# Performance work log

Hardware: AMD Instinct MI355X
Metric: run time of the kernel (lower is better)

Reference implementation:

```python
import jax, jax.numpy as jnp
import numpy as np

EMBED_DIM = 1024
NUM_HEADS = 16
HEAD_DIM = EMBED_DIM // NUM_HEADS


def setup_inputs() -> dict:
    key = jax.random.key(0)
    ks = jax.random.split(key, 5)
    B, S, D = 2, 2048, EMBED_DIM
    scale = 1.0 / np.sqrt(D)
    x = jax.random.normal(ks[0], (B, S, D), dtype=jnp.float32)
    qkv_w = jax.random.uniform(ks[1], (3 * D, D), dtype=jnp.float32, minval=-scale, maxval=scale)
    qkv_b = jax.random.uniform(ks[2], (3 * D,), dtype=jnp.float32, minval=-scale, maxval=scale)
    out_w = jax.random.uniform(ks[3], (D, D), dtype=jnp.float32, minval=-scale, maxval=scale)
    out_b = jax.random.uniform(ks[4], (D,), dtype=jnp.float32, minval=-scale, maxval=scale)
    return {"x": x, "qkv_w": qkv_w, "qkv_b": qkv_b, "out_w": out_w, "out_b": out_b}


def reference(x, qkv_w, qkv_b, out_w, out_b):
    B, S, D = x.shape
    H, hd = NUM_HEADS, HEAD_DIM
    # QKV projection (torch Linear: y = x @ W^T + b)
    qkv = jnp.einsum('bsd,ed->bse', x, qkv_w) + qkv_b          # [B,S,3D]
    qkv = qkv.reshape(B, S, 3, H, hd)
    q, k, v = (jnp.moveaxis(qkv[:, :, i], 2, 1) for i in range(3))  # each [B,H,S,hd]
    scores = jnp.einsum('bhqd,bhkd->bhqk', q, k) / np.sqrt(hd)  # [B,H,S,S]
    probs = jax.nn.softmax(scores, axis=-1)
    attn = jnp.einsum('bhqk,bhkd->bhqd', probs, v)              # [B,H,S,hd]
    attn = jnp.moveaxis(attn, 1, 2).reshape(B, S, D)
    return jnp.einsum('bsd,ed->bse', attn, out_w) + out_b
```

## Files before the change

kernel.cpp:

```cpp
#include <hip/hip_runtime.h>
#include <stdint.h>

typedef __bf16 bf16;
typedef __attribute__((ext_vector_type(2))) __bf16 bf16x2;
typedef __attribute__((ext_vector_type(4))) __bf16 bf16x4;
typedef __attribute__((ext_vector_type(8))) __bf16 bf16x8;
typedef __attribute__((ext_vector_type(4))) float f32x4;
typedef __attribute__((ext_vector_type(16))) float f32x16;

#define LOG2E_OVER_8 0.18033688011112042f

#if __has_builtin(__builtin_amdgcn_exp2f)
#define EXP2(x) __builtin_amdgcn_exp2f(x)
#else
#define EXP2(x) exp2f(x)
#endif

__device__ __forceinline__ void gl_lds16(const bf16* g, bf16* l) {
  __builtin_amdgcn_global_load_lds(
      (const __attribute__((address_space(1))) void*)g,
      (__attribute__((address_space(3))) void*)l, 16, 0, 0);
}
#define WAIT_VM0_BARRIER() asm volatile("s_waitcnt vmcnt(0)\n\ts_barrier" ::: "memory")

__device__ __forceinline__ uint32_t pack2(float a, float b) {
  union { bf16x2 v; uint32_t u; } z;
  z.v[0] = (bf16)a; z.v[1] = (bf16)b;
  return z.u;
}

__device__ __forceinline__ void pl32swap(uint32_t& a, uint32_t& b) {
  asm("v_permlane32_swap_b32 %0, %1" : "+v"(a), "+v"(b));
}

#define N_X  (4096 * 1024)
#define N_WQ (3072 * 1024)
#define N_WO (1024 * 1024)
__global__ __launch_bounds__(256) void cvt3_kernel(const float* __restrict__ x,
                                                   const float* __restrict__ wq,
                                                   const float* __restrict__ wo,
                                                   bf16* __restrict__ d) {
  int i = (blockIdx.x * 256 + threadIdx.x) * 8;
  const float* s;
  if (i < N_X) s = x + i;
  else if (i < N_X + N_WQ) s = wq + (i - N_X);
  else s = wo + (i - N_X - N_WQ);
  float4 a = *(const float4*)s;
  float4 b = *(const float4*)(s + 4);
  bf16x8 o;
  o[0] = (bf16)a.x; o[1] = (bf16)a.y; o[2] = (bf16)a.z; o[3] = (bf16)a.w;
  o[4] = (bf16)b.x; o[5] = (bf16)b.y; o[6] = (bf16)b.z; o[7] = (bf16)b.w;
  *(bf16x8*)(d + i) = o;
}

template <int EPI>
__global__ __launch_bounds__(256, 3) void gemm_bt(
    const bf16* __restrict__ A, const bf16* __restrict__ Bw,
    const float* __restrict__ bias,
    bf16* __restrict__ qo, bf16* __restrict__ ko, bf16* __restrict__ vTo,
    float* __restrict__ outF) {
  constexpr int MT = EPI ? 64 : 128;
  constexpr int MI = MT / 32;
  constexpr int BK = EPI ? 64 : 32;
  constexpr int NC = BK / 32;
  constexpr int NIT = 1024 / BK;
  constexpr int ASZ = MT * BK;
  constexpr int BSZ = 128 * BK;
  constexpr int RS = 136;
  constexpr int SME0 = 2 * ASZ + 2 * BSZ;
  constexpr int SME = EPI ? SME0 : (SME0 > 128 * RS ? SME0 : 128 * RS);
  __shared__ __attribute__((aligned(16))) bf16 smem[SME];

  int bx, by;
  {
    const int f = blockIdx.x;
    const int xcd = f & 7, idx = f >> 3;
    if constexpr (EPI == 0) { by = xcd * 4 + (idx & 3); bx = idx >> 2; }
    else                    { by = xcd * 8 + (idx & 7); bx = idx >> 3; }
  }

  const int t = threadIdx.x;
  const int L = t & 63;
  const int li = L & 15;
  const int qd = L >> 4;
  const int w = t >> 6;
  const int wm = (w >> 1) * (MT / 2);
  const int wn = (w & 1) * 64;
  const int bm0 = by * MT;
  const int bn0 = bx * 128;
  const int r_st = t >> 2;
  const int c_st = (t & 3) * 8;

  const bf16* Ab = A + (size_t)bm0 * 1024;
  const bf16* Bb = Bw + (size_t)bn0 * 1024;

  auto issue = [&](int k0, int bi) {
    bf16* As_ = smem + bi * ASZ;
    bf16* Bs_ = smem + 2 * ASZ + bi * BSZ;
#pragma unroll
    for (int kc = 0; kc < NC; ++kc) {
      const int kk = k0 + kc * 32;
      gl_lds16(Ab + (size_t)r_st * 1024 + kk + c_st, As_ + kc * MT * 32 + t * 8);
      if constexpr (MT == 128)
        gl_lds16(Ab + (size_t)(r_st + 64) * 1024 + kk + c_st,
                 As_ + kc * MT * 32 + (t + 256) * 8);
      gl_lds16(Bb + (size_t)r_st * 1024 + kk + c_st, Bs_ + kc * 4096 + t * 8);
      gl_lds16(Bb + (size_t)(r_st + 64) * 1024 + kk + c_st,
               Bs_ + kc * 4096 + (t + 256) * 8);
    }
  };

  f32x4 acc[MI][4] = {};
  issue(0, 0);
  for (int it = 0; it < NIT; ++it) {
    WAIT_VM0_BARRIER();
    if (it < NIT - 1) issue((it + 1) * BK, (it + 1) & 1);
    const bf16* Ac = smem + (it & 1) * ASZ;
    const bf16* Bc = smem + 2 * ASZ + (it & 1) * BSZ;
#pragma unroll
    for (int kc = 0; kc < NC; ++kc) {
      const bf16* Ak = Ac + kc * MT * 32;
      const bf16* Bk = Bc + kc * 4096;
      bf16x8 af[MI], bfr[4];
#pragma unroll
      for (int mi = 0; mi < MI; ++mi)
        af[mi] = *(const bf16x8*)(Ak + (wm + mi * 16 + li) * 32 + qd * 8);
#pragma unroll
      for (int ni = 0; ni < 4; ++ni)
        bfr[ni] = *(const bf16x8*)(Bk + (wn + ni * 16 + li) * 32 + qd * 8);
#pragma unroll
      for (int mi = 0; mi < MI; ++mi)
#pragma unroll
        for (int ni = 0; ni < 4; ++ni)
          acc[mi][ni] = __builtin_amdgcn_mfma_f32_16x16x32_bf16(
              af[mi], bfr[ni], acc[mi][ni], 0, 0, 0);
    }
  }

  if constexpr (EPI == 0) {
    const int which = bn0 >> 10;
    __syncthreads();
    bf16* Ct = smem;
    if (which == 2) {
#pragma unroll
      for (int mi = 0; mi < MI; ++mi) {
        const int m_l = wm + mi * 16 + qd * 4;
#pragma unroll
        for (int ni = 0; ni < 4; ++ni) {
          const int n_l = wn + ni * 16 + li;
          const float bi = bias[bn0 + n_l];
          bf16x4 pk;
#pragma unroll
          for (int r = 0; r < 4; ++r) pk[r] = (bf16)(acc[mi][ni][r] + bi);
          *(bf16x4*)(Ct + n_l * RS + m_l) = pk;
        }
      }
    } else {
      const float sc = (which == 0) ? LOG2E_OVER_8 : 1.0f;
#pragma unroll
      for (int mi = 0; mi < MI; ++mi) {
        const int m_l = wm + mi * 16 + qd * 4;
#pragma unroll
        for (int ni = 0; ni < 4; ++ni) {
          const int n_l = wn + ni * 16 + li;
          const float bi = bias[bn0 + n_l];
#pragma unroll
          for (int r = 0; r < 4; ++r)
            Ct[(m_l + r) * RS + n_l] = (bf16)((acc[mi][ni][r] + bi) * sc);
        }
      }
    }
    __syncthreads();
    const int jr = t >> 4;
    const int jc = t & 15;
#pragma unroll
    for (int pass = 0; pass < 8; ++pass) {
      const int row = pass * 16 + jr;
      bf16x8 vv = *(const bf16x8*)(Ct + row * RS + jc * 8);
      if (which == 2) {
        const int n_g = bn0 + row;
        const int hh = (n_g >> 6) & 15, dd = n_g & 63;
        const int bb = bm0 >> 11;
        const int s_b = (bm0 & 2047) + jc * 8;
        *(bf16x8*)(vTo + ((size_t)(bb * 16 + hh) * 64 + dd) * 2048 + s_b) = vv;
      } else {
        const int m_g = bm0 + row;
        const int bb = m_g >> 11, ss = m_g & 2047;
        const int n_g = bn0 + jc * 8;
        const int hh = (n_g >> 6) & 15, dd = n_g & 63;
        bf16* dst = (which == 0 ? qo : ko);
        *(bf16x8*)(dst + ((size_t)(bb * 16 + hh) * 2048 + ss) * 64 + dd) = vv;
      }
    }
  } else {
#pragma unroll
    for (int mi = 0; mi < MI; ++mi) {
      const int m_g = bm0 + wm + mi * 16 + qd * 4;
#pragma unroll
      for (int ni = 0; ni < 4; ++ni) {
        const int n_g = bn0 + wn + ni * 16 + li;
        const float bi = bias[n_g];
#pragma unroll
        for (int r = 0; r < 4; ++r)
          outF[(size_t)(m_g + r) * 1024 + n_g] = acc[mi][ni][r] + bi;
      }
    }
  }
}

__global__ __launch_bounds__(512, 2) void attn_fwd(
    const bf16* __restrict__ Q, const bf16* __restrict__ K,
    const bf16* __restrict__ VT, bf16* __restrict__ AO) {
  __shared__ __attribute__((aligned(16))) bf16 smem[65536];
  const int t = threadIdx.x;
  const int half = t >> 8;
  const int tt = t & 255;
  const int L = t & 63;
  const int m31 = L & 31;
  const int hi = (L >> 5) & 1;
  const int w = (t >> 6) & 3;

  const int lid = blockIdx.x;
  const int bh_ = ((lid & 7) << 2) + (lid >> 6);
  const int qb = (lid >> 3) & 7;
  const int b = bh_ >> 4, h = bh_ & 15;
  const size_t bh = (size_t)(b * 16 + h);

  const bf16* Qp = Q + bh * 2048 * 64;
  const bf16* Kp = K + bh * 2048 * 64 + (size_t)half * 1024 * 64;
  const bf16* Vp = VT + bh * 64 * 2048 + half * 1024;
  const int q0 = qb * 256 + w * 64;

  bf16x8 qf[2][4];
#pragma unroll
  for (int qs = 0; qs < 2; ++qs)
#pragma unroll
    for (int s = 0; s < 4; ++s)
      qf[qs][s] = *(const bf16x8*)(
          Qp + (size_t)(q0 + qs * 32 + m31) * 64 + s * 16 + hi * 8);

  f32x16 acc[2][2] = {};
  f32x16 accS[2] = {};

  union FU { uint32_t u[4]; bf16x8 v; };
  FU onesf;
  onesf.u[0] = 0x3F803F80u; onesf.u[1] = 0x3F803F80u;
  onesf.u[2] = 0x3F803F80u; onesf.u[3] = 0x3F803F80u;

  bf16* Kbase = smem + half * 32768;
  bf16* Vbase = Kbase + 16384;

  const int srow = tt >> 3;
  const int scc = (tt & 7) ^ (srow & 7);
  auto issue = [&](int it2, int bi) {
#pragma unroll
    for (int tile = 0; tile < 2; ++tile) {
      const int kt = it2 * 2 + tile;
      const bf16* Kt = Kp + (size_t)kt * 4096;
      const bf16* Vt = Vp + kt * 64;
      bf16* Kd = Kbase + bi * 8192 + tile * 4096;
      bf16* Vd = Vbase + bi * 8192 + tile * 4096;
#pragma unroll
      for (int r = 0; r < 2; ++r) {
        gl_lds16(Kt + (srow + 32 * r) * 64 + scc * 8, Kd + (tt + 256 * r) * 8);
        gl_lds16(Vt + (size_t)(srow + 32 * r) * 2048 + scc * 8, Vd + (tt + 256 * r) * 8);
      }
    }
  };

  const int rlow = m31 & 7;

  auto SM = [&](const f32x16& st, FU* afp) {
    uint32_t pk[8];
#pragma unroll
    for (int j = 0; j < 8; ++j) {
      float a = EXP2(st[2 * j]);
      float c = EXP2(st[2 * j + 1]);
      pk[j] = pack2(a, c);
    }
    pl32swap(pk[0], pk[2]);
    pl32swap(pk[1], pk[3]);
    pl32swap(pk[4], pk[6]);
    pl32swap(pk[5], pk[7]);
    afp[0].u[0] = pk[0]; afp[0].u[1] = pk[1];
    afp[0].u[2] = pk[2]; afp[0].u[3] = pk[3];
    afp[1].u[0] = pk[4]; afp[1].u[1] = pk[5];
    afp[1].u[2] = pk[6]; afp[1].u[3] = pk[7];
  };

  issue(0, 0);
  for (int it2 = 0; it2 < 8; ++it2) {
    WAIT_VM0_BARRIER();
    if (it2 < 7) issue(it2 + 1, (it2 + 1) & 1);
    const bf16* Kc0 = Kbase + (it2 & 1) * 8192;
    const bf16* Vc0 = Vbase + (it2 & 1) * 8192;

    bf16x8 kfa[4][4];
#pragma unroll
    for (int kt = 0; kt < 4; ++kt)
#pragma unroll
      for (int s = 0; s < 4; ++s)
        kfa[kt][s] = *(const bf16x8*)(
            Kc0 + (kt >> 1) * 4096 +
            (((kt & 1) * 32 + m31) * 8 + ((2 * s + hi) ^ rlow)) * 8);
    __builtin_amdgcn_sched_barrier(0);

#pragma unroll
    for (int kt = 0; kt < 4; ++kt) {
      f32x16 st2[2];
      __builtin_amdgcn_s_setprio(1);
#pragma unroll
      for (int qs = 0; qs < 2; ++qs) {
        f32x16 z = {};
#pragma unroll
        for (int s = 0; s < 4; ++s)
          z = __builtin_amdgcn_mfma_f32_32x32x16_bf16(kfa[kt][s], qf[qs][s], z,
                                                      0, 0, 0);
        st2[qs] = z;
      }
      __builtin_amdgcn_s_setprio(0);

      bf16x8 vfa[2][2];
#pragma unroll
      for (int dt = 0; dt < 2; ++dt)
#pragma unroll
        for (int u = 0; u < 2; ++u)
          vfa[dt][u] = *(const bf16x8*)(
              Vc0 + (kt >> 1) * 4096 +
              ((dt * 32 + m31) * 8 + (((kt & 1) * 4 + u * 2 + hi) ^ rlow)) * 8);
      __builtin_amdgcn_sched_barrier(0);

      FU A[2][2];
      SM(st2[0], A[0]);
      SM(st2[1], A[1]);

      __builtin_amdgcn_s_setprio(1);
#pragma unroll
      for (int qs = 0; qs < 2; ++qs)
#pragma unroll
        for (int u = 0; u < 2; ++u)
          accS[qs] = __builtin_amdgcn_mfma_f32_32x32x16_bf16(
              A[qs][u].v, onesf.v, accS[qs], 0, 0, 0);
#pragma unroll
      for (int dt = 0; dt < 2; ++dt)
#pragma unroll
        for (int u = 0; u < 2; ++u)
#pragma unroll
          for (int qs = 0; qs < 2; ++qs)
            acc[dt][qs] = __builtin_amdgcn_mfma_f32_32x32x16_bf16(
                A[qs][u].v, vfa[dt][u], acc[dt][qs], 0, 0, 0);
      __builtin_amdgcn_s_setprio(0);
    }
  }

  __syncthreads();
  float* xch = (float*)smem;
  const int slot = w * 64 + L;
  float* rec = xch + (size_t)slot * 97;
  if (half == 1) {
#pragma unroll
    for (int dt = 0; dt < 2; ++dt)
#pragma unroll
      for (int qs = 0; qs < 2; ++qs)
#pragma unroll
        for (int r = 0; r < 16; ++r)
          rec[dt * 32 + qs * 16 + r] = acc[dt][qs][r];
#pragma unroll
    for (int qs = 0; qs < 2; ++qs)
#pragma unroll
      for (int r = 0; r < 16; ++r)
        rec[64 + qs * 16 + r] = accS[qs][r];
  }
  __syncthreads();
  if (half == 0) {
#pragma unroll
    for (int dt = 0; dt < 2; ++dt)
#pragma unroll
      for (int qs = 0; qs < 2; ++qs)
#pragma unroll
        for (int r = 0; r < 16; ++r)
          acc[dt][qs][r] += rec[dt * 32 + qs * 16 + r];
#pragma unroll
    for (int qs = 0; qs < 2; ++qs)
#pragma unroll
      for (int r = 0; r < 16; ++r)
        accS[qs][r] += rec[64 + qs * 16 + r];

#pragma unroll
    for (int qs = 0; qs < 2; ++qs)
#pragma unroll
      for (int r = 0; r < 16; ++r) {
        const int qrow = (r & 3) + 8 * (r >> 2) + 4 * hi;
        const float invq = 1.f / accS[qs][r];
        const size_t base =
            ((size_t)b * 2048 + q0 + qs * 32 + qrow) * 1024 + h * 64 + m31;
        AO[base] = (bf16)(acc[0][qs][r] * invq);
        AO[base + 32] = (bf16)(acc[1][qs][r] * invq);
      }
  }
}

extern "C" void kernel_launch(void* const* d_in, const int* in_sizes, int n_in,
                              void* d_out, int out_size, void* d_ws, size_t ws_size,
                              hipStream_t stream) {
  const float* x = (const float*)d_in[0];
  const float* qkvw = (const float*)d_in[1];
  const float* qkvb = (const float*)d_in[2];
  const float* outw = (const float*)d_in[3];
  const float* outb = (const float*)d_in[4];
  float* out = (float*)d_out;

  bf16* xb = (bf16*)d_ws;
  bf16* wq = xb + (size_t)N_X;
  bf16* wo = wq + (size_t)N_WQ;
  bf16* q = wo + (size_t)N_WO;
  bf16* kk = q + (size_t)2 * 16 * 2048 * 64;
  bf16* vT = kk + (size_t)2 * 16 * 2048 * 64;
  bf16* attn = xb;

  cvt3_kernel<<<4096, 256, 0, stream>>>(x, qkvw, outw, xb);

  gemm_bt<0><<<768, 256, 0, stream>>>(xb, wq, qkvb, q, kk, vT, nullptr);
  attn_fwd<<<256, 512, 0, stream>>>(q, kk, vT, attn);
  gemm_bt<1><<<512, 256, 0, stream>>>(attn, wo, outb, nullptr, nullptr, nullptr, out);
}
```

Before: 176.6 us.

## Replace QKV projection GEMM with 256x256-tile 512-thread kernel

Adds a dedicated QKV GEMM kernel using 256x256 output tiles with 8 waves, double-buffered direct global-to-LDS loads, and an XCD-aware block mapping, launched as 192 blocks instead of 768 smaller ones. The epilogue writes Q/K/V^T in slabs through LDS to fit the larger tile. The goal is higher arithmetic intensity and less redundant operand traffic. The cost is only 192 blocks, which may underfill the GPU's compute units, plus heavy register use from 128 accumulators per thread and extra barriers in the slab epilogue.

```diff
diff --git a/kernel.cpp b/kernel.cpp
--- a/kernel.cpp
+++ b/kernel.cpp
@@ -138,60 +138,6 @@
   }
 
   if constexpr (EPI == 0) {
-    const int which = bn0 >> 10;
-    __syncthreads();
-    bf16* Ct = smem;
-    if (which == 2) {
-#pragma unroll
-      for (int mi = 0; mi < MI; ++mi) {
-        const int m_l = wm + mi * 16 + qd * 4;
-#pragma unroll
-        for (int ni = 0; ni < 4; ++ni) {
-          const int n_l = wn + ni * 16 + li;
-          const float bi = bias[bn0 + n_l];
-          bf16x4 pk;
-#pragma unroll
-          for (int r = 0; r < 4; ++r) pk[r] = (bf16)(acc[mi][ni][r] + bi);
-          *(bf16x4*)(Ct + n_l * RS + m_l) = pk;
-        }
-      }
-    } else {
-      const float sc = (which == 0) ? LOG2E_OVER_8 : 1.0f;
-#pragma unroll
-      for (int mi = 0; mi < MI; ++mi) {
-        const int m_l = wm + mi * 16 + qd * 4;
-#pragma unroll
-        for (int ni = 0; ni < 4; ++ni) {
-          const int n_l = wn + ni * 16 + li;
-          const float bi = bias[bn0 + n_l];
-#pragma unroll
-          for (int r = 0; r < 4; ++r)
-            Ct[(m_l + r) * RS + n_l] = (bf16)((acc[mi][ni][r] + bi) * sc);
-        }
-      }
-    }
-    __syncthreads();
-    const int jr = t >> 4;
-    const int jc = t & 15;
-#pragma unroll
-    for (int pass = 0; pass < 8; ++pass) {
-      const int row = pass * 16 + jr;
-      bf16x8 vv = *(const bf16x8*)(Ct + row * RS + jc * 8);
-      if (which == 2) {
-        const int n_g = bn0 + row;
-        const int hh = (n_g >> 6) & 15, dd = n_g & 63;
-        const int bb = bm0 >> 11;
-        const int s_b = (bm0 & 2047) + jc * 8;
-        *(bf16x8*)(vTo + ((size_t)(bb * 16 + hh) * 64 + dd) * 2048 + s_b) = vv;
-      } else {
-        const int m_g = bm0 + row;
-        const int bb = m_g >> 11, ss = m_g & 2047;
-        const int n_g = bn0 + jc * 8;
-        const int hh = (n_g >> 6) & 15, dd = n_g & 63;
-        bf16* dst = (which == 0 ? qo : ko);
-        *(bf16x8*)(dst + ((size_t)(bb * 16 + hh) * 2048 + ss) * 64 + dd) = vv;
-      }
-    }
   } else {
 #pragma unroll
     for (int mi = 0; mi < MI; ++mi) {
@@ -203,6 +149,140 @@
 #pragma unroll
         for (int r = 0; r < 4; ++r)
           outF[(size_t)(m_g + r) * 1024 + n_g] = acc[mi][ni][r] + bi;
+      }
+    }
+  }
+}
+
+__global__ __launch_bounds__(512, 2) void gemm256(
+    const bf16* __restrict__ A, const bf16* __restrict__ Bw,
+    const float* __restrict__ bias,
+    bf16* __restrict__ qo, bf16* __restrict__ ko, bf16* __restrict__ vTo) {
+  constexpr int BK = 32;
+  constexpr int NIT = 32;
+  constexpr int ASZ = 256 * BK;
+  constexpr int BSZ = 256 * BK;
+  constexpr int RS2 = 264;
+  __shared__ __attribute__((aligned(16))) bf16 smem[2 * ASZ + 2 * BSZ];
+
+  const int f = blockIdx.x;
+  const int xcd = f & 7, idx = f >> 3;
+  const int by = xcd * 2 + (idx & 1);
+  const int bx = idx >> 1;
+
+  const int t = threadIdx.x;
+  const int L = t & 63;
+  const int li = L & 15;
+  const int qd = L >> 4;
+  const int w = t >> 6;
+  const int wm = (w >> 2) * 128;
+  const int wn = (w & 3) * 64;
+  const int bm0 = by * 256;
+  const int bn0 = bx * 256;
+  const int r_st = t >> 2;
+  const int c_st = (t & 3) * 8;
+
+  const bf16* Ab = A + (size_t)bm0 * 1024;
+  const bf16* Bb = Bw + (size_t)bn0 * 1024;
+
+  auto issue = [&](int kk, int bi) {
+    bf16* As_ = smem + bi * ASZ;
+    bf16* Bs_ = smem + 2 * ASZ + bi * BSZ;
+    gl_lds16(Ab + (size_t)r_st * 1024 + kk + c_st, As_ + t * 8);
+    gl_lds16(Ab + (size_t)(r_st + 128) * 1024 + kk + c_st, As_ + (t + 512) * 8);
+    gl_lds16(Bb + (size_t)r_st * 1024 + kk + c_st, Bs_ + t * 8);
+    gl_lds16(Bb + (size_t)(r_st + 128) * 1024 + kk + c_st, Bs_ + (t + 512) * 8);
+  };
+
+  f32x4 acc[8][4] = {};
+  issue(0, 0);
+  for (int it = 0; it < NIT; ++it) {
+    WAIT_VM0_BARRIER();
+    if (it < NIT - 1) issue((it + 1) * BK, (it + 1) & 1);
+    const bf16* Ak = smem + (it & 1) * ASZ;
+    const bf16* Bk = smem + 2 * ASZ + (it & 1) * BSZ;
+    bf16x8 af[8], bfr[4];
+#pragma unroll
+    for (int mi = 0; mi < 8; ++mi)
+      af[mi] = *(const bf16x8*)(Ak + (wm + mi * 16 + li) * 32 + qd * 8);
+#pragma unroll
+    for (int ni = 0; ni < 4; ++ni)
+      bfr[ni] = *(const bf16x8*)(Bk + (wn + ni * 16 + li) * 32 + qd * 8);
+#pragma unroll
+    for (int mi = 0; mi < 8; ++mi)
+#pragma unroll
+      for (int ni = 0; ni < 4; ++ni)
+        acc[mi][ni] = __builtin_amdgcn_mfma_f32_16x16x32_bf16(
+            af[mi], bfr[ni], acc[mi][ni], 0, 0, 0);
+  }
+
+  const int which = bn0 >> 10;
+  bf16* Ct = smem;
+  if (which != 2) {
+    const float sc = (which == 0) ? LOG2E_OVER_8 : 1.0f;
+    bf16* dst = (which == 0) ? qo : ko;
+#pragma unroll
+    for (int slab = 0; slab < 4; ++slab) {
+      __syncthreads();
+      if ((wm >> 7) == (slab >> 1)) {
+        const int mib = (slab & 1) * 4;
+#pragma unroll
+        for (int mi2 = 0; mi2 < 4; ++mi2) {
+          const int mi = mib + mi2;
+          const int lr = mi2 * 16 + qd * 4;
+#pragma unroll
+          for (int ni = 0; ni < 4; ++ni) {
+            const int n_l = wn + ni * 16 + li;
+            const float bi = bias[bn0 + n_l];
+#pragma unroll
+            for (int r = 0; r < 4; ++r)
+              Ct[(lr + r) * RS2 + n_l] = (bf16)((acc[mi][ni][r] + bi) * sc);
+          }
+        }
+      }
+      __syncthreads();
+      const int row = t >> 3;
+      const int m_g = bm0 + slab * 64 + row;
+      const int bb = m_g >> 11, ss = m_g & 2047;
+#pragma unroll
+      for (int p = 0; p < 4; ++p) {
+        const int c8 = (t & 7) + p * 8;
+        bf16x8 vv = *(const bf16x8*)(Ct + row * RS2 + c8 * 8);
+        const int n_g = bn0 + c8 * 8;
+        const int hh = (n_g >> 6) & 15, dd = n_g & 63;
+        *(bf16x8*)(dst + ((size_t)(bb * 16 + hh) * 2048 + ss) * 64 + dd) = vv;
+      }
+    }
+  } else {
+#pragma unroll
+    for (int slab = 0; slab < 4; ++slab) {
+      __syncthreads();
+      if ((w & 3) == slab) {
+#pragma unroll
+        for (int ni = 0; ni < 4; ++ni) {
+          const int nl = ni * 16 + li;
+          const float bi = bias[bn0 + slab * 64 + nl];
+#pragma unroll
+          for (int mi = 0; mi < 8; ++mi) {
+            const int m_l = wm + mi * 16 + qd * 4;
+            bf16x4 pk;
+#pragma unroll
+            for (int r = 0; r < 4; ++r) pk[r] = (bf16)(acc[mi][ni][r] + bi);
+            *(bf16x4*)(Ct + nl * RS2 + m_l) = pk;
+          }
+        }
+      }
+      __syncthreads();
+      const int row = t >> 3;
+      const int n_g = bn0 + slab * 64 + row;
+      const int hh = (n_g >> 6) & 15, dd = n_g & 63;
+      const int bb = bm0 >> 11;
+#pragma unroll
+      for (int p = 0; p < 4; ++p) {
+        const int c8 = (t & 7) + p * 8;
+        bf16x8 vv = *(const bf16x8*)(Ct + row * RS2 + c8 * 8);
+        const int s_b = (bm0 & 2047) + c8 * 8;
+        *(bf16x8*)(vTo + ((size_t)(bb * 16 + hh) * 64 + dd) * 2048 + s_b) = vv;
       }
     }
   }
@@ -420,7 +500,7 @@
 
   cvt3_kernel<<<4096, 256, 0, stream>>>(x, qkvw, outw, xb);
 
-  gemm_bt<0><<<768, 256, 0, stream>>>(xb, wq, qkvb, q, kk, vT, nullptr);
+  gemm256<<<192, 512, 0, stream>>>(xb, wq, qkvb, q, kk, vT);
   attn_fwd<<<256, 512, 0, stream>>>(q, kk, vT, attn);
   gemm_bt<1><<<512, 256, 0, stream>>>(attn, wo, outb, nullptr, nullptr, nullptr, out);
 }
```

Result: no change. 176.4 us (-0.1%).
